# Optimization experiments

Measured on AMD Instinct MI355X. Metric: run time of the kernel, lower is better.

The kernel has to match this reference:

```python
import math
import jax
import jax.numpy as jnp
import numpy as np

WH, WW = 8, 8
DIM, NUM_HEADS = 768, 24
CPB_HIDDEN = 512


def _rel_tables(Wh, Ww):
    # relative_position_index: (N, N) int, values in [0, (2Wh-1)*(2Ww-1))
    coords = np.stack(np.meshgrid(np.arange(Wh), np.arange(Ww), indexing='ij')).reshape(2, -1)
    rel = coords[:, :, None] - coords[:, None, :]          # (2, N, N)
    rel = rel.transpose(1, 2, 0).astype(np.int64)          # (N, N, 2)
    rel[:, :, 0] += Wh - 1
    rel[:, :, 1] += Ww - 1
    rel[:, :, 0] *= 2 * Ww - 1
    idx = rel.sum(-1)                                      # (N, N)
    # relative_coords_table: ((2Wh-1)*(2Ww-1), 2), log-spaced CPB coords
    rch = np.arange(-(Wh - 1), Wh, dtype=np.float32)
    rcw = np.arange(-(Ww - 1), Ww, dtype=np.float32)
    table = np.stack(np.meshgrid(rch, rcw, indexing='ij')).transpose(1, 2, 0).reshape(-1, 2)
    table[:, 0] /= max(Wh - 1, 1)
    table[:, 1] /= max(Ww - 1, 1)
    table *= 8.0
    table = np.sign(table) * np.log2(np.abs(table) + 1.0) / math.log2(8.0)
    return idx.astype(np.int32), table.astype(np.float32)


def setup_inputs() -> dict:
    key = jax.random.key(0)
    ks = jax.random.split(key, 8)
    B_, N, C = 1024, WH * WW, DIM
    idx, table = _rel_tables(WH, WW)
    return {
        'x': jax.random.normal(ks[0], (B_, N, C), dtype=jnp.float32),
        'qkv_w': jax.random.normal(ks[1], (C, 3 * C), dtype=jnp.float32) * 0.02,
        'qkv_b': jnp.zeros((3 * C,), dtype=jnp.float32),
        'proj_w': jax.random.normal(ks[2], (C, C), dtype=jnp.float32) * 0.02,
        'proj_b': jnp.zeros((C,), dtype=jnp.float32),
        'cpb_w1': jax.random.normal(ks[3], (2, CPB_HIDDEN), dtype=jnp.float32) * 0.1,
        'cpb_b1': jnp.zeros((CPB_HIDDEN,), dtype=jnp.float32),
        'cpb_w2': jax.random.normal(ks[4], (CPB_HIDDEN, NUM_HEADS), dtype=jnp.float32) * 0.05,
        'logit_scale': jnp.full((NUM_HEADS, 1, 1), math.log(10.0), dtype=jnp.float32),
        'rel_coords_table': jnp.asarray(table),
        'rel_pos_index': jnp.asarray(idx),
    }


def reference(x, qkv_w, qkv_b, proj_w, proj_b, cpb_w1, cpb_b1, cpb_w2,
              logit_scale, rel_coords_table, rel_pos_index):
    B_, N, C = x.shape
    H = logit_scale.shape[0]
    hd = C // H
    qkv = (x @ qkv_w + qkv_b).reshape(B_, N, 3, H, hd).transpose(2, 0, 3, 1, 4)
    q, k, v = qkv[0], qkv[1], qkv[2]                        # (B_, H, N, hd)
    # cosine attention: L2-normalize q, k (eps as in F.normalize)
    q = q / jnp.maximum(jnp.linalg.norm(q, axis=-1, keepdims=True), 1e-12)
    k = k / jnp.maximum(jnp.linalg.norm(k, axis=-1, keepdims=True), 1e-12)
    ls = jnp.exp(jnp.minimum(logit_scale, math.log(1.0 / 0.01)))  # (H,1,1)
    q = q * ls
    # CPB bias: MLP over rel coords table, gather by relative_position_index
    bias_table = jnp.maximum(rel_coords_table @ cpb_w1 + cpb_b1, 0.0) @ cpb_w2  # (T, H)
    bias = bias_table[rel_pos_index.reshape(-1)].reshape(N, N, H).transpose(2, 0, 1)[None]  # (1,H,N,N)
    attn = jnp.einsum('bhnd,bhmd->bhnm', q, k) + bias      # scale = 1.0
    attn = jax.nn.softmax(attn, axis=-1)
    out = jnp.einsum('bhnm,bhmd->bhnd', attn, v)
    out = out.transpose(0, 2, 1, 3).reshape(B_, N, C)
    return out @ proj_w + proj_b
```

## Files before the change

### kernel.cpp

```cpp
#include <hip/hip_runtime.h>
#include <hip/hip_bf16.h>

typedef __bf16 bf16_t;
typedef __bf16 bf16x8 __attribute__((ext_vector_type(8)));
typedef __bf16 bf16x4 __attribute__((ext_vector_type(4)));
typedef float f32x4 __attribute__((ext_vector_type(4)));

static __device__ __forceinline__ f32x4 mfma16(bf16x8 a, bf16x8 b, f32x4 c) {
  return __builtin_amdgcn_mfma_f32_16x16x32_bf16(a, b, c, 0, 0, 0);
}

static __device__ __forceinline__ void gload16(const bf16_t* g, bf16_t* l) {
  __builtin_amdgcn_global_load_lds(
      (const __attribute__((address_space(1))) void*)g,
      (__attribute__((address_space(3))) void*)l, 16, 0, 0);
}

__global__ __launch_bounds__(256) void cvt_bf16_kernel(
    const float* __restrict__ in, bf16_t* __restrict__ out, int n8) {
  int i = blockIdx.x * 256 + threadIdx.x;
  int stride = gridDim.x * 256;
  for (; i < n8; i += stride) {
    float4 a = ((const float4*)in)[2 * i];
    float4 b = ((const float4*)in)[2 * i + 1];
    bf16x8 w = {(bf16_t)a.x, (bf16_t)a.y, (bf16_t)a.z, (bf16_t)a.w,
                (bf16_t)b.x, (bf16_t)b.y, (bf16_t)b.z, (bf16_t)b.w};
    ((bf16x8*)out)[i] = w;
  }
}

__global__ __launch_bounds__(256) void transpose_cvt_kernel(
    const float* __restrict__ W, bf16_t* __restrict__ WT, int K, int N) {
  __shared__ float tile[32][33];
  int n0 = blockIdx.x * 32, k0 = blockIdx.y * 32;
  int tx = threadIdx.x & 31, ty = threadIdx.x >> 5;
#pragma unroll
  for (int i = 0; i < 32; i += 8)
    tile[ty + i][tx] = W[(size_t)(k0 + ty + i) * N + n0 + tx];
  __syncthreads();
#pragma unroll
  for (int i = 0; i < 32; i += 8)
    WT[(size_t)(n0 + ty + i) * K + k0 + tx] = (bf16_t)tile[tx][ty + i];
}

__global__ __launch_bounds__(512) void cpb_table_kernel(
    const float* __restrict__ table, const float* __restrict__ w1,
    const float* __restrict__ b1, const float* __restrict__ w2,
    float* __restrict__ bias_table) {
  __shared__ float hbuf[512];
  int t = blockIdx.x;
  int j = threadIdx.x;
  float c0 = table[2 * t], c1 = table[2 * t + 1];
  float h = c0 * w1[j] + c1 * w1[512 + j] + b1[j];
  hbuf[j] = h > 0.f ? h : 0.f;
  __syncthreads();
  int wave = j >> 6, lane = j & 63;
  for (int hh = wave * 3; hh < wave * 3 + 3; ++hh) {
    float s = 0.f;
    for (int jj = lane; jj < 512; jj += 64) s += hbuf[jj] * w2[jj * 24 + hh];
    for (int off = 32; off > 0; off >>= 1) s += __shfl_down(s, off, 64);
    if (lane == 0) bias_table[t * 24 + hh] = s;
  }
}

__global__ __launch_bounds__(256) void bias_expand_kernel(
    const float* __restrict__ bias_table, const int* __restrict__ idx,
    float* __restrict__ bias) {
  int h = blockIdx.x;
  for (int nm = threadIdx.x; nm < 4096; nm += 256)
    bias[h * 4096 + nm] = bias_table[idx[nm] * 24 + h];
}

template <int EPI, int NCOLS>
__global__ __launch_bounds__(256) void gemm_kernel(
    const bf16_t* __restrict__ A, const bf16_t* __restrict__ BT,
    const float* __restrict__ bias, void* __restrict__ outp, int K) {
  constexpr int NT = NCOLS / 128;
  __shared__ bf16_t As[2][4096];
  __shared__ bf16_t Bs[2][4096];
  int tid = threadIdx.x;
  int wave = tid >> 6, lane = tid & 63;
  int wrow = (wave >> 1) * 64, wcol = (wave & 1) * 64;
  int cpx = gridDim.x >> 3;
  int wg = (blockIdx.x & 7) * cpx + (blockIdx.x >> 3);
  int mt = wg / NT, nt = wg % NT;
  int m0 = mt * 128, n0 = nt * 128;

  const bf16_t* Abase = A + (size_t)(m0 + (tid >> 2)) * K + (tid & 3) * 8;
  const bf16_t* Bbase = BT + (size_t)(n0 + (tid >> 2)) * K + (tid & 3) * 8;
  size_t rstep = (size_t)64 * K;

  auto stage = [&](int bufi, int kt) {
    const bf16_t* a = Abase + kt * 32;
    const bf16_t* b = Bbase + kt * 32;
    gload16(a, &As[bufi][tid * 8]);
    gload16(a + rstep, &As[bufi][tid * 8 + 2048]);
    gload16(b, &Bs[bufi][tid * 8]);
    gload16(b + rstep, &Bs[bufi][tid * 8 + 2048]);
  };

  f32x4 acc[4][4] = {};
  int nk = K / 32;
  stage(0, 0);
  for (int kt = 0; kt < nk; ++kt) {
    __syncthreads();
    if (kt + 1 < nk) stage((kt + 1) & 1, kt + 1);
    int bufi = kt & 1;
    int hi8 = (lane >> 4) * 8;
    bf16x8 af[4], bfr[4];
#pragma unroll
    for (int mr = 0; mr < 4; ++mr)
      af[mr] = *(const bf16x8*)&As[bufi][(wrow + mr * 16 + (lane & 15)) * 32 + hi8];
#pragma unroll
    for (int nc = 0; nc < 4; ++nc)
      bfr[nc] = *(const bf16x8*)&Bs[bufi][(wcol + nc * 16 + (lane & 15)) * 32 + hi8];
#pragma unroll
    for (int mr = 0; mr < 4; ++mr)
#pragma unroll
      for (int nc = 0; nc < 4; ++nc)
        acc[mr][nc] = mfma16(af[mr], bfr[nc], acc[mr][nc]);
  }

  int hi4 = (lane >> 4) * 4;
  if constexpr (EPI == 0) {
    bf16_t* out = (bf16_t*)outp;
    int sidx = n0 / 768;
#pragma unroll
    for (int mr = 0; mr < 4; ++mr)
#pragma unroll
      for (int nc = 0; nc < 4; ++nc) {
        int gcol = n0 + wcol + nc * 16 + (lane & 15);
        int within = gcol - sidx * 768;
        int h = within >> 5, d = within & 31;
        float bv = bias[gcol];
#pragma unroll
        for (int j = 0; j < 4; ++j) {
          int grow = m0 + wrow + mr * 16 + hi4 + j;
          int bwin = grow >> 6, nn = grow & 63;
          size_t off = ((((size_t)sidx * 1024 + bwin) * 24 + h) * 64 + nn) * 32 + d;
          out[off] = (bf16_t)(acc[mr][nc][j] + bv);
        }
      }
  } else {
    float* out = (float*)outp;
#pragma unroll
    for (int mr = 0; mr < 4; ++mr)
#pragma unroll
      for (int nc = 0; nc < 4; ++nc) {
        int gcol = n0 + wcol + nc * 16 + (lane & 15);
        float bv = bias[gcol];
#pragma unroll
        for (int j = 0; j < 4; ++j) {
          int grow = m0 + wrow + mr * 16 + hi4 + j;
          out[(size_t)grow * NCOLS + gcol] = acc[mr][nc][j] + bv;
        }
      }
  }
}

__global__ __launch_bounds__(64) void attn_kernel(
    const bf16_t* __restrict__ qkv, const float* __restrict__ bias,
    const float* __restrict__ logit_scale, bf16_t* __restrict__ attn_out) {
  __shared__ __align__(16) char smem[14848];
  bf16_t (*qs)[40] = (bf16_t(*)[40])smem;
  bf16_t (*kk)[40] = (bf16_t(*)[40])(smem + 5120);
  bf16_t (*vT)[72] = (bf16_t(*)[72])(smem + 10240);
  bf16_t (*ps)[72] = (bf16_t(*)[72])smem;
  int h = blockIdx.x >> 10;
  int b = blockIdx.x & 1023;
  int lane = threadIdx.x;
  float ls = __expf(fminf(logit_scale[h], 4.6051701859880914f));
  size_t base = ((size_t)b * 24 + h) * 2048;
  const bf16_t* qrow = qkv + base + lane * 32;
  const bf16_t* krow = qkv + (size_t)50331648 + base + lane * 32;
  const bf16_t* vrow = qkv + (size_t)100663296 + base + lane * 32;
  {
    bf16x8 r[4];
#pragma unroll
    for (int i = 0; i < 4; ++i) r[i] = *(const bf16x8*)(qrow + i * 8);
    float f[32], sq = 0.f;
#pragma unroll
    for (int i = 0; i < 4; ++i)
#pragma unroll
      for (int j = 0; j < 8; ++j) { float x = (float)r[i][j]; f[i * 8 + j] = x; sq += x * x; }
    float sc = ls / fmaxf(sqrtf(sq), 1e-12f);
#pragma unroll
    for (int i = 0; i < 4; ++i) {
      bf16x8 w;
#pragma unroll
      for (int j = 0; j < 8; ++j) w[j] = (bf16_t)(f[i * 8 + j] * sc);
      *(bf16x8*)&qs[lane][i * 8] = w;
    }
  }
  {
    bf16x8 r[4];
#pragma unroll
    for (int i = 0; i < 4; ++i) r[i] = *(const bf16x8*)(krow + i * 8);
    float f[32], sq = 0.f;
#pragma unroll
    for (int i = 0; i < 4; ++i)
#pragma unroll
      for (int j = 0; j < 8; ++j) { float x = (float)r[i][j]; f[i * 8 + j] = x; sq += x * x; }
    float sc = 1.f / fmaxf(sqrtf(sq), 1e-12f);
#pragma unroll
    for (int i = 0; i < 4; ++i) {
      bf16x8 w;
#pragma unroll
      for (int j = 0; j < 8; ++j) w[j] = (bf16_t)(f[i * 8 + j] * sc);
      *(bf16x8*)&kk[lane][i * 8] = w;
    }
  }
  {
    bf16x8 r[4];
#pragma unroll
    for (int i = 0; i < 4; ++i) r[i] = *(const bf16x8*)(vrow + i * 8);
#pragma unroll
    for (int i = 0; i < 4; ++i)
#pragma unroll
      for (int j = 0; j < 8; ++j) vT[i * 8 + j][lane] = r[i][j];
  }
  __syncthreads();
  f32x4 sacc[4][4] = {};
  {
    bf16x8 qa[4], kb[4];
#pragma unroll
    for (int mr = 0; mr < 4; ++mr)
      qa[mr] = *(bf16x8*)&qs[mr * 16 + (lane & 15)][(lane >> 4) * 8];
#pragma unroll
    for (int nc = 0; nc < 4; ++nc)
      kb[nc] = *(bf16x8*)&kk[nc * 16 + (lane & 15)][(lane >> 4) * 8];
#pragma unroll
    for (int mr = 0; mr < 4; ++mr)
#pragma unroll
      for (int nc = 0; nc < 4; ++nc)
        sacc[mr][nc] = mfma16(qa[mr], kb[nc], sacc[mr][nc]);
  }
  const float* bh = bias + h * 4096;
  int hi4 = (lane >> 4) * 4;
#pragma unroll
  for (int mr = 0; mr < 4; ++mr)
#pragma unroll
    for (int j = 0; j < 4; ++j) {
      int r = mr * 16 + hi4 + j;
      float v0 = sacc[mr][0][j] + bh[r * 64 + 0 + (lane & 15)];
      float v1 = sacc[mr][1][j] + bh[r * 64 + 16 + (lane & 15)];
      float v2 = sacc[mr][2][j] + bh[r * 64 + 32 + (lane & 15)];
      float v3 = sacc[mr][3][j] + bh[r * 64 + 48 + (lane & 15)];
      float m = fmaxf(fmaxf(v0, v1), fmaxf(v2, v3));
#pragma unroll
      for (int off = 1; off < 16; off <<= 1) m = fmaxf(m, __shfl_xor(m, off, 64));
      v0 = __expf(v0 - m); v1 = __expf(v1 - m);
      v2 = __expf(v2 - m); v3 = __expf(v3 - m);
      float sum = v0 + v1 + v2 + v3;
#pragma unroll
      for (int off = 1; off < 16; off <<= 1) sum += __shfl_xor(sum, off, 64);
      float inv = 1.f / sum;
      ps[r][0 + (lane & 15)] = (bf16_t)(v0 * inv);
      ps[r][16 + (lane & 15)] = (bf16_t)(v1 * inv);
      ps[r][32 + (lane & 15)] = (bf16_t)(v2 * inv);
      ps[r][48 + (lane & 15)] = (bf16_t)(v3 * inv);
    }
  __syncthreads();
  f32x4 oacc[4][2] = {};
#pragma unroll
  for (int ks_ = 0; ks_ < 2; ++ks_) {
    bf16x8 pa[4], vb[2];
#pragma unroll
    for (int mr = 0; mr < 4; ++mr)
      pa[mr] = *(bf16x8*)&ps[mr * 16 + (lane & 15)][ks_ * 32 + (lane >> 4) * 8];
#pragma unroll
    for (int c2 = 0; c2 < 2; ++c2)
      vb[c2] = *(bf16x8*)&vT[c2 * 16 + (lane & 15)][ks_ * 32 + (lane >> 4) * 8];
#pragma unroll
    for (int mr = 0; mr < 4; ++mr)
#pragma unroll
      for (int c2 = 0; c2 < 2; ++c2)
        oacc[mr][c2] = mfma16(pa[mr], vb[c2], oacc[mr][c2]);
  }
#pragma unroll
  for (int mr = 0; mr < 4; ++mr)
#pragma unroll
    for (int c2 = 0; c2 < 2; ++c2) {
      int d = c2 * 16 + (lane & 15);
#pragma unroll
      for (int j = 0; j < 4; ++j) {
        int r = mr * 16 + hi4 + j;
        attn_out[((size_t)b * 64 + r) * 768 + h * 32 + d] = (bf16_t)oacc[mr][c2][j];
      }
    }
}

extern "C" void kernel_launch(void* const* d_in, const int* in_sizes, int n_in,
                              void* d_out, int out_size, void* d_ws, size_t ws_size,
                              hipStream_t stream) {
  const float* x = (const float*)d_in[0];
  const float* qkv_w = (const float*)d_in[1];
  const float* qkv_b = (const float*)d_in[2];
  const float* proj_w = (const float*)d_in[3];
  const float* proj_b = (const float*)d_in[4];
  const float* cpb_w1 = (const float*)d_in[5];
  const float* cpb_b1 = (const float*)d_in[6];
  const float* cpb_w2 = (const float*)d_in[7];
  const float* logit_scale = (const float*)d_in[8];
  const float* rel_tab = (const float*)d_in[9];
  const int* rel_idx = (const int*)d_in[10];

  char* ws = (char*)d_ws;
  float* bias_table = (float*)ws;
  float* bias = (float*)(ws + 32768);
  bf16_t* wTq = (bf16_t*)(ws + 425984);
  bf16_t* wTp = (bf16_t*)(ws + 3964928);
  bf16_t* qkv = (bf16_t*)(ws + 5144576);
  bf16_t* xb = (bf16_t*)(ws + 307134464);
  bf16_t* attn = xb;

  cvt_bf16_kernel<<<2048, 256, 0, stream>>>(x, xb, 6291456);
  transpose_cvt_kernel<<<dim3(72, 24), 256, 0, stream>>>(qkv_w, wTq, 768, 2304);
  transpose_cvt_kernel<<<dim3(24, 24), 256, 0, stream>>>(proj_w, wTp, 768, 768);
  cpb_table_kernel<<<225, 512, 0, stream>>>(rel_tab, cpb_w1, cpb_b1, cpb_w2, bias_table);
  bias_expand_kernel<<<24, 256, 0, stream>>>(bias_table, rel_idx, bias);
  gemm_kernel<0, 2304><<<9216, 256, 0, stream>>>(xb, wTq, qkv_b, qkv, 768);
  attn_kernel<<<24576, 64, 0, stream>>>(qkv, bias, logit_scale, attn);
  gemm_kernel<1, 768><<<3072, 256, 0, stream>>>(attn, wTp, proj_b, d_out, 768);
}
```

Before: 655.4 us.

## Enlarge GEMM tiles to 256x256 with swizzled LDS and split-phase pipelining

The two projection GEMMs move from 128x128 tiles with 4 waves to 256x256 tiles with 8 waves per block. LDS is XOR-swizzled to avoid bank conflicts, and a hand-scheduled double buffer issues the B and A loads in separate phases, using explicit waitcnt, barriers and setprio around the MFMA groups. The goal is more operand reuse per byte loaded and better overlap of global-to-LDS copies with MFMA work. In exchange, each wave holds 128 accumulator floats, which raises register pressure and may limit occupancy. The fixed K template and the fewer, larger blocks also mean less parallelism for the proj GEMM (768 blocks).

```diff
diff --git a/kernel.cpp b/kernel.cpp
--- a/kernel.cpp
+++ b/kernel.cpp
@@ -3,18 +3,23 @@
 
 typedef __bf16 bf16_t;
 typedef __bf16 bf16x8 __attribute__((ext_vector_type(8)));
-typedef __bf16 bf16x4 __attribute__((ext_vector_type(4)));
 typedef float f32x4 __attribute__((ext_vector_type(4)));
 
 static __device__ __forceinline__ f32x4 mfma16(bf16x8 a, bf16x8 b, f32x4 c) {
   return __builtin_amdgcn_mfma_f32_16x16x32_bf16(a, b, c, 0, 0, 0);
 }
 
-static __device__ __forceinline__ void gload16(const bf16_t* g, bf16_t* l) {
+static __device__ __forceinline__ void gload16(const void* g, void* l) {
   __builtin_amdgcn_global_load_lds(
       (const __attribute__((address_space(1))) void*)g,
       (__attribute__((address_space(3))) void*)l, 16, 0, 0);
 }
+
+#define BAR() __builtin_amdgcn_s_barrier()
+#define SCHED0() __builtin_amdgcn_sched_barrier(0)
+#define WAITVM2() do { asm volatile("s_waitcnt vmcnt(2)" ::: "memory"); SCHED0(); } while (0)
+#define WAITVM0() do { asm volatile("s_waitcnt vmcnt(0)" ::: "memory"); SCHED0(); } while (0)
+#define WAITLGKM0() do { asm volatile("s_waitcnt lgkmcnt(0)" ::: "memory"); SCHED0(); } while (0)
 
 __global__ __launch_bounds__(256) void cvt_bf16_kernel(
     const float* __restrict__ in, bf16_t* __restrict__ out, int n8) {
@@ -71,54 +76,80 @@
     bias[h * 4096 + nm] = bias_table[idx[nm] * 24 + h];
 }
 
-template <int EPI, int NCOLS>
-__global__ __launch_bounds__(256) void gemm_kernel(
+#define MFMA_QUAD(MRLO)                                          \
+  do {                                                           \
+    _Pragma("unroll") for (int mr = 0; mr < 4; ++mr)             \
+        _Pragma("unroll") for (int nc = 0; nc < 4; ++nc)         \
+            acc[MRLO + mr][nc] =                                 \
+        mfma16(af[MRLO + mr], bfr[nc], acc[MRLO + mr][nc]);      \
+  } while (0)
+
+template <int EPI, int NCOLS, int K>
+__global__ __launch_bounds__(512, 2) void gemm_kernel(
     const bf16_t* __restrict__ A, const bf16_t* __restrict__ BT,
-    const float* __restrict__ bias, void* __restrict__ outp, int K) {
-  constexpr int NT = NCOLS / 128;
-  __shared__ bf16_t As[2][4096];
-  __shared__ bf16_t Bs[2][4096];
+    const float* __restrict__ bias, void* __restrict__ outp) {
+  constexpr int NT = NCOLS / 256;
+  constexpr int Kb = K * 2;
+  constexpr int nk = K / 32;
+  __shared__ __align__(16) char lds[65536];
   int tid = threadIdx.x;
   int wave = tid >> 6, lane = tid & 63;
-  int wrow = (wave >> 1) * 64, wcol = (wave & 1) * 64;
+  int wm = wave >> 2, wn = wave & 3;
   int cpx = gridDim.x >> 3;
   int wg = (blockIdx.x & 7) * cpx + (blockIdx.x >> 3);
   int mt = wg / NT, nt = wg % NT;
-  int m0 = mt * 128, n0 = nt * 128;
-
-  const bf16_t* Abase = A + (size_t)(m0 + (tid >> 2)) * K + (tid & 3) * 8;
-  const bf16_t* Bbase = BT + (size_t)(n0 + (tid >> 2)) * K + (tid & 3) * 8;
-  size_t rstep = (size_t)64 * K;
-
-  auto stage = [&](int bufi, int kt) {
-    const bf16_t* a = Abase + kt * 32;
-    const bf16_t* b = Bbase + kt * 32;
-    gload16(a, &As[bufi][tid * 8]);
-    gload16(a + rstep, &As[bufi][tid * 8 + 2048]);
-    gload16(b, &Bs[bufi][tid * 8]);
-    gload16(b + rstep, &Bs[bufi][tid * 8 + 2048]);
-  };
-
-  f32x4 acc[4][4] = {};
-  int nk = K / 32;
-  stage(0, 0);
-  for (int kt = 0; kt < nk; ++kt) {
-    __syncthreads();
-    if (kt + 1 < nk) stage((kt + 1) & 1, kt + 1);
-    int bufi = kt & 1;
-    int hi8 = (lane >> 4) * 8;
-    bf16x8 af[4], bfr[4];
-#pragma unroll
-    for (int mr = 0; mr < 4; ++mr)
-      af[mr] = *(const bf16x8*)&As[bufi][(wrow + mr * 16 + (lane & 15)) * 32 + hi8];
+  int m0 = mt * 256, n0 = nt * 256;
+
+  int wST = ((tid & 63) * 16);
+  wST ^= (((wST >> 9) & 1) << 5);
+  int srow = ((tid >> 6) << 4) + (wST >> 6);
+  int scolb = wST & 63;
+  const char* Asrc = (const char*)A + (size_t)(m0 + srow) * Kb + scolb;
+  const char* Bsrc = (const char*)BT + (size_t)(n0 + srow) * Kb + scolb;
+  char* Adst = lds + tid * 16;
+  char* Bdst = lds + 32768 + tid * 16;
+
+  int rr = lane & 15;
+  int wRD = (rr * 64 + ((lane >> 4) * 16)) ^ (((rr >> 3) & 1) << 5);
+  const char* aRd = lds + wm * 8192 + wRD;
+  const char* bRd = lds + 32768 + (wn >> 1) * 8192 + (wn & 1) * 4096 + wRD;
+
+#define STAGE_A(BUF, H, KT) \
+  gload16(Asrc + (size_t)(H)*128 * Kb + (size_t)(KT)*64, Adst + ((BUF) << 14) + ((H) << 13))
+#define STAGE_B(BUF, H, KT) \
+  gload16(Bsrc + (size_t)(H)*128 * Kb + (size_t)(KT)*64, Bdst + ((BUF) << 14) + ((H) << 13))
+
+  f32x4 acc[8][4] = {};
+  STAGE_A(0, 0, 0); STAGE_A(0, 1, 0);
+  STAGE_B(0, 0, 0); STAGE_B(0, 1, 0);
+  STAGE_A(1, 0, 1); STAGE_A(1, 1, 1);
+  WAITVM2();
+  BAR(); SCHED0();
+
+  for (int t = 0; t < nk; ++t) {
+    int buf = t & 1;
+    int bufo = buf << 14;
+    if (t + 1 < nk) { STAGE_B(buf ^ 1, 0, t + 1); STAGE_B(buf ^ 1, 1, t + 1); }
+    bf16x8 af[8], bfr[4];
+#pragma unroll
+    for (int mr = 0; mr < 8; ++mr)
+      af[mr] = *(const bf16x8*)(aRd + bufo + mr * 1024);
 #pragma unroll
     for (int nc = 0; nc < 4; ++nc)
-      bfr[nc] = *(const bf16x8*)&Bs[bufi][(wcol + nc * 16 + (lane & 15)) * 32 + hi8];
-#pragma unroll
-    for (int mr = 0; mr < 4; ++mr)
-#pragma unroll
-      for (int nc = 0; nc < 4; ++nc)
-        acc[mr][nc] = mfma16(af[mr], bfr[nc], acc[mr][nc]);
+      bfr[nc] = *(const bf16x8*)(bRd + bufo + nc * 1024);
+    BAR(); SCHED0();
+    __builtin_amdgcn_s_setprio(1);
+    MFMA_QUAD(0);
+    __builtin_amdgcn_s_setprio(0);
+    WAITLGKM0();
+    BAR(); SCHED0();
+    if (t + 2 < nk) { STAGE_A(buf, 0, t + 2); STAGE_A(buf, 1, t + 2); }
+    __builtin_amdgcn_s_setprio(1);
+    MFMA_QUAD(4);
+    __builtin_amdgcn_s_setprio(0);
+    if (t + 2 < nk) { WAITVM2(); }
+    else if (t + 1 < nk) { WAITVM0(); }
+    if (t + 1 < nk) { BAR(); SCHED0(); }
   }
 
   int hi4 = (lane >> 4) * 4;
@@ -126,16 +157,16 @@
     bf16_t* out = (bf16_t*)outp;
     int sidx = n0 / 768;
 #pragma unroll
-    for (int mr = 0; mr < 4; ++mr)
+    for (int mr = 0; mr < 8; ++mr)
 #pragma unroll
       for (int nc = 0; nc < 4; ++nc) {
-        int gcol = n0 + wcol + nc * 16 + (lane & 15);
+        int gcol = n0 + wn * 64 + nc * 16 + (lane & 15);
         int within = gcol - sidx * 768;
         int h = within >> 5, d = within & 31;
         float bv = bias[gcol];
 #pragma unroll
         for (int j = 0; j < 4; ++j) {
-          int grow = m0 + wrow + mr * 16 + hi4 + j;
+          int grow = m0 + wm * 128 + mr * 16 + hi4 + j;
           int bwin = grow >> 6, nn = grow & 63;
           size_t off = ((((size_t)sidx * 1024 + bwin) * 24 + h) * 64 + nn) * 32 + d;
           out[off] = (bf16_t)(acc[mr][nc][j] + bv);
@@ -144,14 +175,14 @@
   } else {
     float* out = (float*)outp;
 #pragma unroll
-    for (int mr = 0; mr < 4; ++mr)
+    for (int mr = 0; mr < 8; ++mr)
 #pragma unroll
       for (int nc = 0; nc < 4; ++nc) {
-        int gcol = n0 + wcol + nc * 16 + (lane & 15);
+        int gcol = n0 + wn * 64 + nc * 16 + (lane & 15);
         float bv = bias[gcol];
 #pragma unroll
         for (int j = 0; j < 4; ++j) {
-          int grow = m0 + wrow + mr * 16 + hi4 + j;
+          int grow = m0 + wm * 128 + mr * 16 + hi4 + j;
           out[(size_t)grow * NCOLS + gcol] = acc[mr][nc][j] + bv;
         }
       }
@@ -319,7 +350,7 @@
   transpose_cvt_kernel<<<dim3(24, 24), 256, 0, stream>>>(proj_w, wTp, 768, 768);
   cpb_table_kernel<<<225, 512, 0, stream>>>(rel_tab, cpb_w1, cpb_b1, cpb_w2, bias_table);
   bias_expand_kernel<<<24, 256, 0, stream>>>(bias_table, rel_idx, bias);
-  gemm_kernel<0, 2304><<<9216, 256, 0, stream>>>(xb, wTq, qkv_b, qkv, 768);
+  gemm_kernel<0, 2304, 768><<<2304, 512, 0, stream>>>(xb, wTq, qkv_b, qkv);
   attn_kernel<<<24576, 64, 0, stream>>>(qkv, bias, logit_scale, attn);
-  gemm_kernel<1, 768><<<3072, 256, 0, stream>>>(attn, wTp, proj_b, d_out, 768);
-}
+  gemm_kernel<1, 768, 768><<<768, 512, 0, stream>>>(attn, wTp, proj_b, d_out);
+}
```

Result: faster. 583.9 us (-10.9%).
